# Performance work log

Measured on AMD Instinct MI355X. Metric: run time of the kernel, lower is better.

Reference implementation:

```python
import jax, jax.numpy as jnp
import numpy as np

B, T, D = 2, 2048, 1024
H, DH = 16, 64
WINDOW = 256
SCALE = DH ** -0.5


def setup_inputs() -> dict:
    key = jax.random.key(0)
    ks = jax.random.split(key, 5)
    x = jax.random.normal(ks[0], (B, T, D), dtype=jnp.float32)
    # Linear params (y = x @ W + b form)
    w_qkv = jax.random.normal(ks[1], (D, 3 * D), dtype=jnp.float32) * (D ** -0.5)
    b_qkv = jnp.zeros((3 * D,), dtype=jnp.float32)
    w_out = jax.random.normal(ks[2], (D, D), dtype=jnp.float32) * (D ** -0.5)
    b_out = jnp.zeros((D,), dtype=jnp.float32)
    return {"x": x, "w_qkv": w_qkv, "b_qkv": b_qkv, "w_out": w_out, "b_out": b_out}


def reference(x, w_qkv, b_qkv, w_out, b_out):
    Bs, Ts, Ds = x.shape
    qkv = x @ w_qkv + b_qkv  # [B,T,3D]
    q, k, v = jnp.split(qkv, 3, axis=-1)
    # [B,H,T,dh]
    def heads(t):
        return t.reshape(Bs, Ts, H, DH).transpose(0, 2, 1, 3)
    q, k, v = heads(q), heads(k), heads(v)
    scores = jnp.einsum('bhqd,bhkd->bhqk', q, k) * SCALE
    i = jnp.arange(Ts)[:, None]
    j = jnp.arange(Ts)[None, :]
    # allowed: i - WINDOW <= j <= i  (causal + local window)
    allowed = (j <= i) & (j >= i - WINDOW)
    scores = jnp.where(allowed, scores, -jnp.inf)
    attn = jax.nn.softmax(scores, axis=-1)  # dropout is identity in eval
    out = jnp.einsum('bhqk,bhkd->bhqd', attn, v)
    out = out.transpose(0, 2, 1, 3).reshape(Bs, Ts, Ds)
    return out @ w_out + b_out
```

## Files before the change

### kernel.cpp

```cpp
#include <hip/hip_runtime.h>

#define BN 2
#define T_DIM 2048
#define D_DIM 1024
#define H_N 16
#define DH_N 64
#define WIN 256
#define NROWS (BN * T_DIM)
#define KDIM 1024

typedef __attribute__((ext_vector_type(8))) short bf16x8;
typedef __attribute__((ext_vector_type(4))) float f32x4;
typedef __attribute__((ext_vector_type(8))) unsigned short ushort8;
typedef __attribute__((ext_vector_type(4))) unsigned short u16x4;

static __device__ __forceinline__ unsigned short f2bf(float f) {
  unsigned int u = __float_as_uint(f);
  unsigned int r = (u + 0x7FFFu + ((u >> 16) & 1u)) >> 16;
  return (unsigned short)r;
}

static __device__ __forceinline__ void gl_lds16(const void* g, void* l) {
  __builtin_amdgcn_global_load_lds(
      (const __attribute__((address_space(1))) unsigned int*)g,
      (__attribute__((address_space(3))) unsigned int*)l, 16, 0, 0);
}

#define MFMA16(a, b, c) __builtin_amdgcn_mfma_f32_16x16x32_bf16(a, b, c, 0, 0, 0)

static __device__ __forceinline__ void transpose_tile(
    const float* __restrict__ src, unsigned short* __restrict__ dst, int R,
    int C, int bx, int by, float* tile ) {
  const int t = threadIdx.x;
  const int bc = bx * 64, br = by * 64;
#pragma unroll
  for (int i = 0; i < 16; ++i) {
    int idx = i * 256 + t;
    int r = idx >> 6, c = idx & 63;
    tile[r * 65 + c] = src[(size_t)(br + r) * C + bc + c];
  }
  __syncthreads();
#pragma unroll
  for (int i = 0; i < 16; ++i) {
    int idx = i * 256 + t;
    int r = idx >> 6, c = idx & 63;
    dst[(size_t)(bc + r) * R + br + c] = f2bf(tile[c * 65 + r]);
  }
}

__global__ __launch_bounds__(256) void convert_all(
    const float* __restrict__ x, const float* __restrict__ w_qkv,
    const float* __restrict__ w_out, unsigned short* __restrict__ xbf,
    unsigned short* __restrict__ wqkvt, unsigned short* __restrict__ woutt) {
  __shared__ float tile[64 * 65];
  const int id = blockIdx.x;
  if (id < 2048) {
    int i = (id * 256 + threadIdx.x) * 8;
    float4 a = *(const float4*)(x + i);
    float4 b = *(const float4*)(x + i + 4);
    ushort8 o;
    o[0] = f2bf(a.x); o[1] = f2bf(a.y); o[2] = f2bf(a.z); o[3] = f2bf(a.w);
    o[4] = f2bf(b.x); o[5] = f2bf(b.y); o[6] = f2bf(b.z); o[7] = f2bf(b.w);
    *(ushort8*)(xbf + i) = o;
  } else if (id < 2816) {
    int j = id - 2048;
    transpose_tile(w_qkv, wqkvt, D_DIM, 3 * D_DIM, j % 48, j / 48, tile);
  } else {
    int j = id - 2816;
    transpose_tile(w_out, woutt, D_DIM, D_DIM, j % 16, j / 16, tile);
  }
}

__global__ __launch_bounds__(256) void gemm_qkv_db(
    const unsigned short* __restrict__ A, const unsigned short* __restrict__ Bt,
    const float* __restrict__ bias, unsigned short* __restrict__ qo,
    unsigned short* __restrict__ ko, unsigned short* __restrict__ vto) {
  __shared__ unsigned short As[2][128 * 64];
  __shared__ unsigned short Bs[2][128 * 64];

  const int tid = threadIdx.x;
  const int w = tid >> 6, l = tid & 63;
  const int wr = w >> 1, wc = w & 1;
  const int l15 = l & 15, kslc = l >> 4;

  const int id = blockIdx.x;
  const int wg = (id & 7) * 96 + (id >> 3);
  const int bx = wg % 24, by = wg / 24;
  const int r0 = by * 128, c0 = bx * 128;

  const unsigned short* Ag = A + (size_t)r0 * KDIM;
  const unsigned short* Bg = Bt + (size_t)c0 * KDIM;

  f32x4 acc[4][4];
#pragma unroll
  for (int i = 0; i < 4; ++i)
#pragma unroll
    for (int j = 0; j < 4; ++j) acc[i][j] = (f32x4){0.f, 0.f, 0.f, 0.f};

  const int grow = tid >> 3;
  const int gcol = (tid & 7) ^ (grow & 7);

#define STG(T, BUF)                                                            \
  do {                                                                         \
    const size_t kk0 = (size_t)(T) * 64;                                       \
    _Pragma("unroll") for (int ch = 0; ch < 4; ++ch) {                         \
      gl_lds16(Ag + (size_t)(ch * 32 + grow) * KDIM + kk0 + gcol * 8,          \
               (char*)&As[BUF][0] + ch * 4096 + w * 1024);                     \
      gl_lds16(Bg + (size_t)(ch * 32 + grow) * KDIM + kk0 + gcol * 8,          \
               (char*)&Bs[BUF][0] + ch * 4096 + w * 1024);                     \
    }                                                                          \
  } while (0)

#define LDA(CB, mi, ks)                                                        \
  (*(const bf16x8*)((const char*)&As[CB][0] +                                  \
                    (wr * 64 + (mi)*16 + l15) * 128 +                          \
                    ((((ks)*4 + kslc) ^ (l15 & 7)) << 4)))
#define LDB(CB, ni, ks)                                                        \
  (*(const bf16x8*)((const char*)&Bs[CB][0] +                                  \
                    (wc * 64 + (ni)*16 + l15) * 128 +                          \
                    ((((ks)*4 + kslc) ^ (l15 & 7)) << 4)))

#define HALF(CB, ks)                                                           \
  do {                                                                         \
    bf16x8 a0 = LDA(CB, 0, ks), a1 = LDA(CB, 1, ks), a2 = LDA(CB, 2, ks),      \
           a3 = LDA(CB, 3, ks);                                                \
    bf16x8 b0 = LDB(CB, 0, ks), b1 = LDB(CB, 1, ks), b2 = LDB(CB, 2, ks),      \
           b3 = LDB(CB, 3, ks);                                                \
    __builtin_amdgcn_s_setprio(1);                                             \
    acc[0][0] = MFMA16(a0, b0, acc[0][0]);                                     \
    acc[0][1] = MFMA16(a0, b1, acc[0][1]);                                     \
    acc[0][2] = MFMA16(a0, b2, acc[0][2]);                                     \
    acc[0][3] = MFMA16(a0, b3, acc[0][3]);                                     \
    acc[1][0] = MFMA16(a1, b0, acc[1][0]);                                     \
    acc[1][1] = MFMA16(a1, b1, acc[1][1]);                                     \
    acc[1][2] = MFMA16(a1, b2, acc[1][2]);                                     \
    acc[1][3] = MFMA16(a1, b3, acc[1][3]);                                     \
    acc[2][0] = MFMA16(a2, b0, acc[2][0]);                                     \
    acc[2][1] = MFMA16(a2, b1, acc[2][1]);                                     \
    acc[2][2] = MFMA16(a2, b2, acc[2][2]);                                     \
    acc[2][3] = MFMA16(a2, b3, acc[2][3]);                                     \
    acc[3][0] = MFMA16(a3, b0, acc[3][0]);                                     \
    acc[3][1] = MFMA16(a3, b1, acc[3][1]);                                     \
    acc[3][2] = MFMA16(a3, b2, acc[3][2]);                                     \
    acc[3][3] = MFMA16(a3, b3, acc[3][3]);                                     \
    __builtin_amdgcn_s_setprio(0);                                             \
  } while (0)

  STG(0, 0);
#pragma unroll 2
  for (int t = 0; t < 15; ++t) {
    const int cb = t & 1;
    asm volatile("s_waitcnt vmcnt(0)" ::: "memory");
    __builtin_amdgcn_s_barrier();
    STG(t + 1, cb ^ 1);
    HALF(cb, 0);
    HALF(cb, 1);
  }
  asm volatile("s_waitcnt vmcnt(0)" ::: "memory");
  __builtin_amdgcn_s_barrier();
  HALF(1, 0);
  HALF(1, 1);
#undef STG
#undef LDA
#undef LDB
#undef HALF

#pragma unroll
  for (int ni = 0; ni < 4; ++ni) {
    const int col0 = c0 + wc * 64 + ni * 16;
    const int which = col0 >> 10;
    const int h = (col0 >> 6) & 15;
    const int dh = (col0 & 63) + l15;
    const float bv = bias[col0 + l15];
#pragma unroll
    for (int mi = 0; mi < 4; ++mi) {
      int row = r0 + wr * 64 + mi * 16 + (l >> 4) * 4;
      int b_ = row >> 11, t0 = row & 2047;
      if (which == 2) {
        u16x4 pk;
#pragma unroll
        for (int j = 0; j < 4; ++j) pk[j] = f2bf(acc[mi][ni][j] + bv);
        *(u16x4*)(vto + ((size_t)(b_ * H_N + h) * DH_N + dh) * T_DIM + t0) = pk;
      } else {
        float mul = (which == 0) ? 0.125f : 1.0f;
        unsigned short* dst = (which == 0) ? qo : ko;
#pragma unroll
        for (int j = 0; j < 4; ++j)
          dst[((size_t)(b_ * H_N + h) * T_DIM + t0 + j) * DH_N + dh] =
              f2bf((acc[mi][ni][j] + bv) * mul);
      }
    }
  }
}

__global__ __launch_bounds__(256) void gemm_out_p4(
    const unsigned short* __restrict__ A, const unsigned short* __restrict__ Bt,
    const float* __restrict__ bias, float* __restrict__ fo) {
  __shared__ unsigned short As[4][4096];
  __shared__ unsigned short Bs[4][4096];

  const int tid = threadIdx.x;
  const int w = tid >> 6, l = tid & 63;
  const int wr = w >> 1, wc = w & 1;
  const int l15 = l & 15, kslc = l >> 4;

  const int id = blockIdx.x;
  const int wg = (id & 7) * 32 + (id >> 3);
  const int bx = wg & 7, by = wg >> 3;
  const int r0 = by * 128, c0 = bx * 128;

  const unsigned short* Ag = A + (size_t)r0 * KDIM;
  const unsigned short* Bg = Bt + (size_t)c0 * KDIM;

  f32x4 acc[4][4];
#pragma unroll
  for (int i = 0; i < 4; ++i)
#pragma unroll
    for (int j = 0; j < 4; ++j) acc[i][j] = (f32x4){0.f, 0.f, 0.f, 0.f};

  const int srow = l >> 2;
  const int srcslot = (l & 3) ^ ((l >> 3) & 3);

#define STAGE_O(T, BUF)                                                        \
  do {                                                                         \
    const size_t kk0 = (size_t)(T) * 32;                                       \
    gl_lds16(Ag + (size_t)(w * 16 + srow) * KDIM + kk0 + srcslot * 8,          \
             (char*)&As[BUF][0] + w * 1024);                                   \
    gl_lds16(Ag + (size_t)(64 + w * 16 + srow) * KDIM + kk0 + srcslot * 8,     \
             (char*)&As[BUF][0] + (4 + w) * 1024);                             \
    gl_lds16(Bg + (size_t)(w * 16 + srow) * KDIM + kk0 + srcslot * 8,          \
             (char*)&Bs[BUF][0] + w * 1024);                                   \
    gl_lds16(Bg + (size_t)(64 + w * 16 + srow) * KDIM + kk0 + srcslot * 8,     \
             (char*)&Bs[BUF][0] + (4 + w) * 1024);                             \
  } while (0)

#define OCOMPUTE(CB)                                                           \
  do {                                                                         \
    bf16x8 af[4], bfr[4];                                                      \
    _Pragma("unroll") for (int mi = 0; mi < 4; ++mi) {                         \
      int row = wr * 64 + mi * 16 + l15;                                       \
      af[mi] = *(const bf16x8*)((const char*)&As[CB][0] + row * 64 +           \
                                ((kslc ^ ((row >> 1) & 3)) << 4));             \
    }                                                                          \
    _Pragma("unroll") for (int ni = 0; ni < 4; ++ni) {                         \
      int row = wc * 64 + ni * 16 + l15;                                       \
      bfr[ni] = *(const bf16x8*)((const char*)&Bs[CB][0] + row * 64 +          \
                                 ((kslc ^ ((row >> 1) & 3)) << 4));            \
    }                                                                          \
    __builtin_amdgcn_s_setprio(1);                                             \
    _Pragma("unroll") for (int mi = 0; mi < 4; ++mi)                           \
        _Pragma("unroll") for (int ni = 0; ni < 4; ++ni) acc[mi][ni] =         \
            MFMA16(af[mi], bfr[ni], acc[mi][ni]);                              \
    __builtin_amdgcn_s_setprio(0);                                             \
  } while (0)

  STAGE_O(0, 0);
  STAGE_O(1, 1);

  for (int t = 0; t < 30; ++t) {
    STAGE_O(t + 2, (t + 2) & 3);
    asm volatile("s_waitcnt vmcnt(8)" ::: "memory");
    __builtin_amdgcn_s_barrier();
    OCOMPUTE(t & 3);
  }
  asm volatile("s_waitcnt vmcnt(4)" ::: "memory");
  __builtin_amdgcn_s_barrier();
  OCOMPUTE(2);
  asm volatile("s_waitcnt vmcnt(0)" ::: "memory");
  __builtin_amdgcn_s_barrier();
  OCOMPUTE(3);
#undef STAGE_O
#undef OCOMPUTE

#pragma unroll
  for (int mi = 0; mi < 4; ++mi) {
#pragma unroll
    for (int ni = 0; ni < 4; ++ni) {
      int row = r0 + wr * 64 + mi * 16 + (l >> 4) * 4;
      int col = c0 + wc * 64 + ni * 16 + l15;
      float bv = bias[col];
#pragma unroll
      for (int j = 0; j < 4; ++j)
        fo[(size_t)(row + j) * D_DIM + col] = acc[mi][ni][j] + bv;
    }
  }
}

__global__ __launch_bounds__(256) void attn_mfma(
    const unsigned short* __restrict__ qbf,
    const unsigned short* __restrict__ kbf,
    const unsigned short* __restrict__ vtbf,
    unsigned short* __restrict__ ctx) {
  __shared__ unsigned short Ks[2][64 * 64];
  __shared__ unsigned short Vs[2][64 * 64];
  const int tid = threadIdx.x;
  const int w = tid >> 6, l = tid & 63;
  const int g = l >> 4, ln = l & 15;
  const int qt = blockIdx.x & 31;
  const int bh = blockIdx.x >> 5;
  const int q0 = qt * 64;
  const int q_abs = q0 + w * 16 + ln;

  const unsigned short* kp = kbf + (size_t)bh * T_DIM * DH_N;
  const unsigned short* vtp = vtbf + (size_t)bh * DH_N * T_DIM;

  bf16x8 qf0, qf1;
  {
    const unsigned short* qp = qbf + ((size_t)bh * T_DIM + q_abs) * DH_N;
    qf0 = *(const bf16x8*)(qp + g * 8);
    qf1 = *(const bf16x8*)(qp + 32 + g * 8);
  }

  const int srow = tid >> 2, sc16a = (tid & 3) ^ (srow & 7);
  const int srow2 = srow + 64 >> 0;
#define KAP(row) \
  (32 * (((row) >> 4) & 1) + 8 * (((row)&15) >> 2) + 4 * ((row) >> 5) + ((row)&3))

#define STAGEKV(KT, BUF)                                                       \
  do {                                                                         \
    _Pragma("unroll") for (int i_ = 0; i_ < 2; ++i_) {                         \
      int chunk = i_ * 256 + tid;                                              \
      int row = chunk >> 3, c16 = chunk & 7;                                   \
      int sc16 = c16 ^ (row & 7);                                              \
      int kap = KAP(row);                                                      \
      gl_lds16(kp + (size_t)((KT) + kap) * DH_N + sc16 * 8,                    \
               (char*)&Ks[BUF][0] + chunk * 16);                               \
      gl_lds16(vtp + (size_t)row * T_DIM + (KT) + sc16 * 8,                    \
               (char*)&Vs[BUF][0] + chunk * 16);                               \
    }                                                                          \
  } while (0)

  f32x4 acc_o[4];
#pragma unroll
  for (int nd = 0; nd < 4; ++nd) acc_o[nd] = (f32x4){0.f, 0.f, 0.f, 0.f};
  float m = -1e30f, lsum = 0.f;

  const int kt_lo = (q0 >= WIN) ? (q0 - WIN) : 0;
  const int nt = ((q0 - kt_lo) >> 6) + 1;

  STAGEKV(kt_lo, 0);
  for (int i = 0; i < nt; ++i) {
    const int cb = i & 1;
    const int kt = kt_lo + i * 64;
    asm volatile("s_waitcnt vmcnt(0)" ::: "memory");
    __builtin_amdgcn_s_barrier();
    if (i + 1 < nt) STAGEKV(kt + 64, cb ^ 1);

    f32x4 sacc[4];
#pragma unroll
    for (int nk = 0; nk < 4; ++nk) sacc[nk] = (f32x4){0.f, 0.f, 0.f, 0.f};
#pragma unroll
    for (int ks = 0; ks < 2; ++ks) {
      bf16x8 qf = ks ? qf1 : qf0;
#pragma unroll
      for (int nk = 0; nk < 4; ++nk) {
        int rrow = nk * 16 + ln;
        int c16 = ks * 4 + g;
        bf16x8 kf = *(const bf16x8*)((const char*)&Ks[cb][0] + rrow * 128 +
                                     ((c16 ^ (rrow & 7)) * 16));
        sacc[nk] = MFMA16(kf, qf, sacc[nk]);
      }
    }

    float p[4][4];
    float tm = -1e30f;
#pragma unroll
    for (int nk = 0; nk < 4; ++nk)
#pragma unroll
      for (int j = 0; j < 4; ++j) {
        int k_abs = kt + 32 * (nk & 1) + 8 * g + 4 * (nk >> 1) + j;
        float s = sacc[nk][j];
        bool ok = (k_abs <= q_abs) && (k_abs + WIN >= q_abs);
        s = ok ? s : -1e30f;
        p[nk][j] = s;
        tm = fmaxf(tm, s);
      }
    tm = fmaxf(tm, __shfl_xor(tm, 16, 64));
    tm = fmaxf(tm, __shfl_xor(tm, 32, 64));
    float mn = fmaxf(m, tm);
    float sc = __expf(m - mn);
    float ps = 0.f;
#pragma unroll
    for (int nk = 0; nk < 4; ++nk)
#pragma unroll
      for (int j = 0; j < 4; ++j) {
        p[nk][j] = __expf(p[nk][j] - mn);
        ps += p[nk][j];
      }
    ps += __shfl_xor(ps, 16, 64);
    ps += __shfl_xor(ps, 32, 64);
    lsum = lsum * sc + ps;
    m = mn;
#pragma unroll
    for (int nd = 0; nd < 4; ++nd) {
      acc_o[nd][0] *= sc; acc_o[nd][1] *= sc;
      acc_o[nd][2] *= sc; acc_o[nd][3] *= sc;
    }

    unsigned int pk[4][2];
#pragma unroll
    for (int nk = 0; nk < 4; ++nk) {
      pk[nk][0] = (unsigned)f2bf(p[nk][0]) | ((unsigned)f2bf(p[nk][1]) << 16);
      pk[nk][1] = (unsigned)f2bf(p[nk][2]) | ((unsigned)f2bf(p[nk][3]) << 16);
    }

#pragma unroll
    for (int ks = 0; ks < 2; ++ks) {
      union { unsigned int d[4]; bf16x8 v; } pf;
      pf.d[0] = pk[ks][0];     pf.d[1] = pk[ks][1];
      pf.d[2] = pk[2 + ks][0]; pf.d[3] = pk[2 + ks][1];
#pragma unroll
      for (int nd = 0; nd < 4; ++nd) {
        int drow = nd * 16 + ln;
        int c16 = ks * 4 + g;
        bf16x8 vf = *(const bf16x8*)((const char*)&Vs[cb][0] + drow * 128 +
                                     ((c16 ^ (drow & 7)) * 16));
        acc_o[nd] = MFMA16(vf, pf.v, acc_o[nd]);
      }
    }
  }
#undef STAGEKV
#undef KAP

  float inv = 1.f / lsum;
  const int b_ = bh >> 4, h = bh & 15;
  unsigned short* op = ctx + ((size_t)b_ * T_DIM + q_abs) * D_DIM + h * DH_N;
#pragma unroll
  for (int nd = 0; nd < 4; ++nd) {
    u16x4 o;
#pragma unroll
    for (int j = 0; j < 4; ++j) o[j] = f2bf(acc_o[nd][j] * inv);
    *(u16x4*)(op + nd * 16 + g * 4) = o;
  }
}

extern "C" void kernel_launch(void* const* d_in, const int* in_sizes, int n_in,
                              void* d_out, int out_size, void* d_ws,
                              size_t ws_size, hipStream_t stream) {
  const float* x = (const float*)d_in[0];
  const float* w_qkv = (const float*)d_in[1];
  const float* b_qkv = (const float*)d_in[2];
  const float* w_out = (const float*)d_in[3];
  const float* b_out = (const float*)d_in[4];
  float* out = (float*)d_out;

  const size_t per = (size_t)BN * H_N * T_DIM * DH_N;
  unsigned short* qbf = (unsigned short*)d_ws;
  unsigned short* kbf = qbf + per;
  unsigned short* vtbf = kbf + per;
  unsigned short* xbf = vtbf + per;
  unsigned short* wqkvt = xbf + (size_t)NROWS * D_DIM;
  unsigned short* woutt = wqkvt + (size_t)3 * D_DIM * D_DIM;
  unsigned short* ctxbf = woutt + (size_t)D_DIM * D_DIM;

  convert_all<<<dim3(3072), dim3(256), 0, stream>>>(x, w_qkv, w_out, xbf,
                                                    wqkvt, woutt);

  gemm_qkv_db<<<dim3(768), dim3(256), 0, stream>>>(xbf, wqkvt, b_qkv, qbf, kbf,
                                                   vtbf);

  attn_mfma<<<dim3(BN * H_N * (T_DIM / 64)), dim3(256), 0, stream>>>(
      qbf, kbf, vtbf, ctxbf);

  gemm_out_p4<<<dim3(256), dim3(256), 0, stream>>>(ctxbf, woutt, b_out, out);
}
```

Measured before the change: 93.51 us.

## Retile QKV GEMM to 256x192 tiles using 32x32x16 MFMA

The QKV projection GEMM moves from 128x128 tiles with a K-step of 64 and 16x16x32 MFMAs to 256x192 tiles with a K-step of 32 and 32x32x16 MFMAs. The grid shrinks from 768 to 256 blocks with an XCD-aware block mapping, and the LDS swizzle and epilogue are adapted to the 32x32 accumulator layout. Larger tiles raise arithmetic intensity per byte staged, and the bigger MFMA needs fewer LDS fragment reads per FLOP. In exchange there are 256 blocks on a 256-CU device (one wave of work), higher register pressure, and twice as many barrier iterations.

```diff
diff --git a/kernel.cpp b/kernel.cpp
--- a/kernel.cpp
+++ b/kernel.cpp
@@ -11,6 +11,7 @@
 
 typedef __attribute__((ext_vector_type(8))) short bf16x8;
 typedef __attribute__((ext_vector_type(4))) float f32x4;
+typedef __attribute__((ext_vector_type(16))) float f32x16;
 typedef __attribute__((ext_vector_type(8))) unsigned short ushort8;
 typedef __attribute__((ext_vector_type(4))) unsigned short u16x4;
 
@@ -27,6 +28,7 @@
 }
 
 #define MFMA16(a, b, c) __builtin_amdgcn_mfma_f32_16x16x32_bf16(a, b, c, 0, 0, 0)
+#define MFMA32(a, b, c) __builtin_amdgcn_mfma_f32_32x32x16_bf16(a, b, c, 0, 0, 0)
 
 static __device__ __forceinline__ void transpose_tile(
     const float* __restrict__ src, unsigned short* __restrict__ dst, int R,
@@ -71,123 +73,130 @@
   }
 }
 
-__global__ __launch_bounds__(256) void gemm_qkv_db(
+__global__ __launch_bounds__(256, 2) void gemm_qkv_32(
     const unsigned short* __restrict__ A, const unsigned short* __restrict__ Bt,
     const float* __restrict__ bias, unsigned short* __restrict__ qo,
     unsigned short* __restrict__ ko, unsigned short* __restrict__ vto) {
-  __shared__ unsigned short As[2][128 * 64];
-  __shared__ unsigned short Bs[2][128 * 64];
+  __shared__ unsigned short As[2][256 * 32];
+  __shared__ unsigned short Bs[2][192 * 32];
 
   const int tid = threadIdx.x;
   const int w = tid >> 6, l = tid & 63;
   const int wr = w >> 1, wc = w & 1;
-  const int l15 = l & 15, kslc = l >> 4;
+  const int l31 = l & 31, lh = l >> 5;
 
   const int id = blockIdx.x;
-  const int wg = (id & 7) * 96 + (id >> 3);
-  const int bx = wg % 24, by = wg / 24;
-  const int r0 = by * 128, c0 = bx * 128;
+  const int xcd = id & 7, i = id >> 3;
+  const int by = (xcd & 3) * 4 + (i & 3);
+  const int bx = (xcd >> 2) * 8 + (i >> 2);
+  const int r0 = by * 256, c0 = bx * 192;
 
   const unsigned short* Ag = A + (size_t)r0 * KDIM;
   const unsigned short* Bg = Bt + (size_t)c0 * KDIM;
 
-  f32x4 acc[4][4];
-#pragma unroll
-  for (int i = 0; i < 4; ++i)
-#pragma unroll
-    for (int j = 0; j < 4; ++j) acc[i][j] = (f32x4){0.f, 0.f, 0.f, 0.f};
-
-  const int grow = tid >> 3;
-  const int gcol = (tid & 7) ^ (grow & 7);
+  f32x16 acc[4][3];
+#pragma unroll
+  for (int mi = 0; mi < 4; ++mi)
+#pragma unroll
+    for (int ni = 0; ni < 3; ++ni)
+#pragma unroll
+      for (int r = 0; r < 16; ++r) acc[mi][ni][r] = 0.f;
 
 #define STG(T, BUF)                                                            \
   do {                                                                         \
-    const size_t kk0 = (size_t)(T) * 64;                                       \
-    _Pragma("unroll") for (int ch = 0; ch < 4; ++ch) {                         \
-      gl_lds16(Ag + (size_t)(ch * 32 + grow) * KDIM + kk0 + gcol * 8,          \
-               (char*)&As[BUF][0] + ch * 4096 + w * 1024);                     \
-      gl_lds16(Bg + (size_t)(ch * 32 + grow) * KDIM + kk0 + gcol * 8,          \
-               (char*)&Bs[BUF][0] + ch * 4096 + w * 1024);                     \
+    const size_t kk0 = (size_t)(T) * 32;                                       \
+    _Pragma("unroll") for (int i_ = 0; i_ < 4; ++i_) {                         \
+      int ci = i_ * 256 + tid;                                                 \
+      int row = ci >> 2, slot = ci & 3;                                        \
+      gl_lds16(Ag + (size_t)row * KDIM + kk0 + ((slot ^ ((row >> 1) & 3)) * 8),\
+               (char*)&As[BUF][0] + ci * 16);                                  \
+    }                                                                          \
+    _Pragma("unroll") for (int i_ = 0; i_ < 3; ++i_) {                         \
+      int ci = i_ * 256 + tid;                                                 \
+      int row = ci >> 2, slot = ci & 3;                                        \
+      gl_lds16(Bg + (size_t)row * KDIM + kk0 + ((slot ^ ((row >> 1) & 3)) * 8),\
+               (char*)&Bs[BUF][0] + ci * 16);                                  \
     }                                                                          \
   } while (0)
 
-#define LDA(CB, mi, ks)                                                        \
+#define LDA32(CB, mi, ks)                                                      \
   (*(const bf16x8*)((const char*)&As[CB][0] +                                  \
-                    (wr * 64 + (mi)*16 + l15) * 128 +                          \
-                    ((((ks)*4 + kslc) ^ (l15 & 7)) << 4)))
-#define LDB(CB, ni, ks)                                                        \
+                    (wr * 128 + (mi)*32 + l31) * 64 +                          \
+                    (((((ks)*2 + lh) ^ (((wr * 128 + (mi)*32 + l31) >> 1) & 3))) \
+                     << 4)))
+#define LDB32(CB, ni, ks)                                                      \
   (*(const bf16x8*)((const char*)&Bs[CB][0] +                                  \
-                    (wc * 64 + (ni)*16 + l15) * 128 +                          \
-                    ((((ks)*4 + kslc) ^ (l15 & 7)) << 4)))
-
-#define HALF(CB, ks)                                                           \
+                    (wc * 96 + (ni)*32 + l31) * 64 +                           \
+                    (((((ks)*2 + lh) ^ (((wc * 96 + (ni)*32 + l31) >> 1) & 3))) \
+                     << 4)))
+
+#define KHALF(CB, ks)                                                          \
   do {                                                                         \
-    bf16x8 a0 = LDA(CB, 0, ks), a1 = LDA(CB, 1, ks), a2 = LDA(CB, 2, ks),      \
-           a3 = LDA(CB, 3, ks);                                                \
-    bf16x8 b0 = LDB(CB, 0, ks), b1 = LDB(CB, 1, ks), b2 = LDB(CB, 2, ks),      \
-           b3 = LDB(CB, 3, ks);                                                \
+    bf16x8 a0 = LDA32(CB, 0, ks), a1 = LDA32(CB, 1, ks), a2 = LDA32(CB, 2, ks),\
+           a3 = LDA32(CB, 3, ks);                                              \
+    bf16x8 b0 = LDB32(CB, 0, ks), b1 = LDB32(CB, 1, ks), b2 = LDB32(CB, 2, ks);\
     __builtin_amdgcn_s_setprio(1);                                             \
-    acc[0][0] = MFMA16(a0, b0, acc[0][0]);                                     \
-    acc[0][1] = MFMA16(a0, b1, acc[0][1]);                                     \
-    acc[0][2] = MFMA16(a0, b2, acc[0][2]);                                     \
-    acc[0][3] = MFMA16(a0, b3, acc[0][3]);                                     \
-    acc[1][0] = MFMA16(a1, b0, acc[1][0]);                                     \
-    acc[1][1] = MFMA16(a1, b1, acc[1][1]);                                     \
-    acc[1][2] = MFMA16(a1, b2, acc[1][2]);                                     \
-    acc[1][3] = MFMA16(a1, b3, acc[1][3]);                                     \
-    acc[2][0] = MFMA16(a2, b0, acc[2][0]);                                     \
-    acc[2][1] = MFMA16(a2, b1, acc[2][1]);                                     \
-    acc[2][2] = MFMA16(a2, b2, acc[2][2]);                                     \
-    acc[2][3] = MFMA16(a2, b3, acc[2][3]);                                     \
-    acc[3][0] = MFMA16(a3, b0, acc[3][0]);                                     \
-    acc[3][1] = MFMA16(a3, b1, acc[3][1]);                                     \
-    acc[3][2] = MFMA16(a3, b2, acc[3][2]);                                     \
-    acc[3][3] = MFMA16(a3, b3, acc[3][3]);                                     \
+    acc[0][0] = MFMA32(a0, b0, acc[0][0]);                                     \
+    acc[0][1] = MFMA32(a0, b1, acc[0][1]);                                     \
+    acc[0][2] = MFMA32(a0, b2, acc[0][2]);                                     \
+    acc[1][0] = MFMA32(a1, b0, acc[1][0]);                                     \
+    acc[1][1] = MFMA32(a1, b1, acc[1][1]);                                     \
+    acc[1][2] = MFMA32(a1, b2, acc[1][2]);                                     \
+    acc[2][0] = MFMA32(a2, b0, acc[2][0]);                                     \
+    acc[2][1] = MFMA32(a2, b1, acc[2][1]);                                     \
+    acc[2][2] = MFMA32(a2, b2, acc[2][2]);                                     \
+    acc[3][0] = MFMA32(a3, b0, acc[3][0]);                                     \
+    acc[3][1] = MFMA32(a3, b1, acc[3][1]);                                     \
+    acc[3][2] = MFMA32(a3, b2, acc[3][2]);                                     \
     __builtin_amdgcn_s_setprio(0);                                             \
   } while (0)
 
   STG(0, 0);
 #pragma unroll 2
-  for (int t = 0; t < 15; ++t) {
+  for (int t = 0; t < 31; ++t) {
     const int cb = t & 1;
     asm volatile("s_waitcnt vmcnt(0)" ::: "memory");
     __builtin_amdgcn_s_barrier();
     STG(t + 1, cb ^ 1);
-    HALF(cb, 0);
-    HALF(cb, 1);
+    KHALF(cb, 0);
+    KHALF(cb, 1);
   }
   asm volatile("s_waitcnt vmcnt(0)" ::: "memory");
   __builtin_amdgcn_s_barrier();
-  HALF(1, 0);
-  HALF(1, 1);
+  KHALF(1, 0);
+  KHALF(1, 1);
 #undef STG
-#undef LDA
-#undef LDB
-#undef HALF
-
-#pragma unroll
-  for (int ni = 0; ni < 4; ++ni) {
-    const int col0 = c0 + wc * 64 + ni * 16;
+#undef LDA32
+#undef LDB32
+#undef KHALF
+
+#pragma unroll
+  for (int ni = 0; ni < 3; ++ni) {
+    const int col0 = c0 + wc * 96 + ni * 32;
     const int which = col0 >> 10;
     const int h = (col0 >> 6) & 15;
-    const int dh = (col0 & 63) + l15;
-    const float bv = bias[col0 + l15];
+    const int dh = (col0 & 63) + l31;
+    const float bv = bias[col0 + l31];
 #pragma unroll
     for (int mi = 0; mi < 4; ++mi) {
-      int row = r0 + wr * 64 + mi * 16 + (l >> 4) * 4;
-      int b_ = row >> 11, t0 = row & 2047;
-      if (which == 2) {
-        u16x4 pk;
-#pragma unroll
-        for (int j = 0; j < 4; ++j) pk[j] = f2bf(acc[mi][ni][j] + bv);
-        *(u16x4*)(vto + ((size_t)(b_ * H_N + h) * DH_N + dh) * T_DIM + t0) = pk;
-      } else {
-        float mul = (which == 0) ? 0.125f : 1.0f;
-        unsigned short* dst = (which == 0) ? qo : ko;
-#pragma unroll
-        for (int j = 0; j < 4; ++j)
-          dst[((size_t)(b_ * H_N + h) * T_DIM + t0 + j) * DH_N + dh] =
-              f2bf((acc[mi][ni][j] + bv) * mul);
+      const int rbase = r0 + wr * 128 + mi * 32 + 4 * lh;
+#pragma unroll
+      for (int q = 0; q < 4; ++q) {
+        int row = rbase + 8 * q;
+        int b_ = row >> 11, t0 = row & 2047;
+        if (which == 2) {
+          u16x4 pk;
+#pragma unroll
+          for (int j = 0; j < 4; ++j) pk[j] = f2bf(acc[mi][ni][q * 4 + j] + bv);
+          *(u16x4*)(vto + ((size_t)(b_ * H_N + h) * DH_N + dh) * T_DIM + t0) = pk;
+        } else {
+          float mul = (which == 0) ? 0.125f : 1.0f;
+          unsigned short* dst = (which == 0) ? qo : ko;
+#pragma unroll
+          for (int j = 0; j < 4; ++j)
+            dst[((size_t)(b_ * H_N + h) * T_DIM + t0 + j) * DH_N + dh] =
+                f2bf((acc[mi][ni][q * 4 + j] + bv) * mul);
+        }
       }
     }
   }
@@ -311,8 +320,6 @@
     qf1 = *(const bf16x8*)(qp + 32 + g * 8);
   }
 
-  const int srow = tid >> 2, sc16a = (tid & 3) ^ (srow & 7);
-  const int srow2 = srow + 64 >> 0;
 #define KAP(row) \
   (32 * (((row) >> 4) & 1) + 8 * (((row)&15) >> 2) + 4 * ((row) >> 5) + ((row)&3))
 
@@ -456,7 +463,7 @@
   convert_all<<<dim3(3072), dim3(256), 0, stream>>>(x, w_qkv, w_out, xbf,
                                                     wqkvt, woutt);
 
-  gemm_qkv_db<<<dim3(768), dim3(256), 0, stream>>>(xbf, wqkvt, b_qkv, qbf, kbf,
+  gemm_qkv_32<<<dim3(256), dim3(256), 0, stream>>>(xbf, wqkvt, b_qkv, qbf, kbf,
                                                    vtbf);
 
   attn_mfma<<<dim3(BN * H_N * (T_DIM / 64)), dim3(256), 0, stream>>>(
```

Result: slower. 102.1 us (+9.2%).
